# Kernel optimization log

Measured on AMD Instinct MI355X. Metric: run time of the kernel, lower is better.

## Reference

```python
import jax, jax.numpy as jnp
import numpy as np
from jax import lax

# Static problem sizes (see shape_source)
B, C, N = 32, 512, 64
SENTS_PER_VIDEO = 4
TARGETS_PER_SENT = 2
S = B * SENTS_PER_VIDEO          # 128 sentences
M = S * TARGETS_PER_SENT         # 256 target moments
P = N * (N + 1) // 2             # 2080 valid proposals (upper-tri mask2d)
T_TEMP = 0.1
MARGIN = 0.0
NEG_IOU = 0.5
K_TOP = 1                        # pos_topk
WEIGHT = 1.0


def setup_inputs() -> dict:
    key = jax.random.key(0)
    k1, k2, k3, k4 = jax.random.split(key, 4)
    return {
        "video_feats": jax.random.normal(k1, (B, C, N, N), jnp.float32),
        "sents_feats": jax.random.normal(k2, (S, C), jnp.float32),
        "num_sentences": jnp.full((B,), SENTS_PER_VIDEO, jnp.int32),
        "num_targets": jnp.full((S,), TARGETS_PER_SENT, jnp.int32),
        "iou2d": jax.random.uniform(k3, (S, N, N), jnp.float32),
        "iou2ds": jax.random.uniform(k4, (M, N, N), jnp.float32),
        "mask2d": jnp.triu(jnp.ones((N, N), bool)),
        "epoch": 0,  # < start_DNS_epoch -> DNS branch skipped
    }


def _log_cross_entropy(pos_scores, all_scores, neg_mask, t, m):
    # Faithful to LogCrossEntropy.forward
    pos_exp = jnp.exp((pos_scores - m) / t)
    neg_exp_sum = jnp.sum(jnp.exp(all_scores / t) * neg_mask, axis=-1)
    loss = -((pos_scores - m) / t - jnp.log(pos_exp + neg_exp_sum))
    return jnp.mean(loss)


def _l2_normalize(x, axis=-1, eps=1e-12):
    n = jnp.linalg.norm(x, axis=axis, keepdims=True)
    return x / jnp.maximum(n, eps)


def reference(video_feats, sents_feats, num_sentences, num_targets,
              iou2d, iou2ds, mask2d, epoch):
    # Compact valid proposals (P is static: upper-triangular mask2d)
    idx = jnp.nonzero(mask2d.reshape(-1), size=P)[0]              # (P,)
    v = video_feats.reshape(B, C, N * N)[:, :, idx]               # (B,C,P)
    v = jnp.transpose(v, (0, 2, 1))                               # (B,P,C)
    iou2d_f = iou2d.reshape(S, N * N)[:, idx]                     # (S,P)
    iou2ds_f = iou2ds.reshape(M, N * N)[:, idx]                   # (M,P)

    v = _l2_normalize(v)
    sents = _l2_normalize(sents_feats)

    scatter_s2v = jnp.repeat(jnp.arange(B), num_sentences, total_repeat_length=S)
    scatter_m2s = jnp.repeat(jnp.arange(S), num_targets, total_repeat_length=M)
    scatter_m2v = scatter_s2v[scatter_m2s]

    # top-K proposals per target moment by IoU
    topk_idx = lax.top_k(iou2ds_f, K_TOP)[1]                      # (M,K)
    topk_v = jnp.take_along_axis(v[scatter_m2v], topk_idx[:, :, None], axis=1)  # (M,K,C)

    # inter-video loss
    inter_video_pos = jnp.einsum('mkc,mc->mk', topk_v, sents[scatter_m2s])  # (M,K)
    inter_video_all = jnp.einsum('mkc,sc->mks', topk_v, sents)              # (M,K,S)
    inter_video_neg_mask = (~jnp.eye(S, dtype=bool))[scatter_m2s][:, None, :]  # (M,1,S)
    loss_inter_video = _log_cross_entropy(
        inter_video_pos, inter_video_all, inter_video_neg_mask, T_TEMP, MARGIN)

    # inter-query loss
    inter_query_pos = inter_video_pos                              # (M,K)
    inter_query_all = (sents @ v.reshape(B * P, C).T)[:, None, :]  # (S,1,B*P)
    # pos_mask: block-diagonal per video, refined by IoU > neg_iou inside own block
    onehot = jnp.eye(B, dtype=bool)[scatter_s2v]                   # (S,B)
    pos_mask = (onehot[:, :, None] & (iou2d_f > NEG_IOU)[:, None, :]).reshape(S, B * P)
    inter_query_neg_mask = (~pos_mask)[:, None, :]                 # (S,1,B*P)
    loss_inter_query = _log_cross_entropy(
        inter_query_pos, inter_query_all[scatter_m2s],
        inter_query_neg_mask[scatter_m2s], T_TEMP, MARGIN)

    total = (loss_inter_video + loss_inter_query) * WEIGHT
    return total, loss_inter_video, loss_inter_query
```

## Files before the change

kernel.cpp:

```cpp
#include <hip/hip_runtime.h>
#include <cstdint>

#define BB 32
#define CC 512
#define NSQ 4096
#define SS 128
#define MM 256
#define PP 2080

#define WS_SN     0
#define WS_SNB    262144
#define WS_IDX    393216
#define WS_IV     401536
#define WS_NEGQ   532608

typedef short bf16x8 __attribute__((ext_vector_type(8)));
typedef float f32x4  __attribute__((ext_vector_type(4)));

__device__ __forceinline__ unsigned short f2bf(float x) {
    unsigned int u = __float_as_uint(x);
    unsigned int r = (u + 0x7fffu + ((u >> 16) & 1u)) >> 16;
    return (unsigned short)r;
}

__global__ void k_prep(const float* __restrict__ sents, float* __restrict__ sn,
                       unsigned short* __restrict__ snb,
                       int* __restrict__ idx, float* __restrict__ negq) {
    const int blk = blockIdx.x, t = threadIdx.x;
    if (blk < 128) {
        __shared__ float red[256];
        const float* row = sents + (size_t)blk * CC;
        float x0 = row[t], x1 = row[t + 256];
        red[t] = x0 * x0 + x1 * x1;
        __syncthreads();
        for (int off = 128; off > 0; off >>= 1) {
            if (t < off) red[t] += red[t + off];
            __syncthreads();
        }
        float rn = 1.0f / fmaxf(sqrtf(red[0]), 1e-12f);
        float y0 = x0 * rn, y1 = x1 * rn;
        sn[(size_t)blk * CC + t]        = y0;
        sn[(size_t)blk * CC + t + 256]  = y1;
        snb[(size_t)blk * CC + t]       = f2bf(y0);
        snb[(size_t)blk * CC + t + 256] = f2bf(y1);
    } else if (blk < 144) {
        int i = (blk - 128) * 256 + t;
        int r = i >> 6, c = i & 63;
        if (c >= r) {
            int p = r * 64 - (r * (r - 1)) / 2 + (c - r);
            idx[p] = i;
        }
    } else {
        if (t < 128) negq[t] = 0.0f;
    }
}

#define BK 64
#define LDK 72

__global__ __launch_bounds__(256)
void k_bigd(const float* __restrict__ video, const unsigned short* __restrict__ snb,
            const float* __restrict__ iou2d, float* __restrict__ negq) {
    __shared__ char smem[36864];
    unsigned short* sA = (unsigned short*)smem;
    unsigned short* vB = (unsigned short*)(smem + 18432);

    const int t    = threadIdx.x;
    const int w    = t >> 6;
    const int lane = t & 63;
    const int q    = lane >> 4;
    const int l15  = lane & 15;

    const int b  = blockIdx.x >> 5;
    const int j0 = (blockIdx.x & 31) * 128;

    const int cg = t & 31;
    const int kr = t >> 5;

    f32x4 acc[2][8];
#pragma unroll
    for (int i = 0; i < 2; i++)
#pragma unroll
        for (int j = 0; j < 8; j++) acc[i][j] = (f32x4){0.f, 0.f, 0.f, 0.f};
    float sq0 = 0.f, sq1 = 0.f, sq2 = 0.f, sq3 = 0.f;

    for (int k0 = 0; k0 < CC; k0 += BK) {
        __syncthreads();
#pragma unroll
        for (int it = 0; it < 4; it++) {
            int lin = t + it * 256;
            int row = lin >> 3, kc = (lin & 7) * 8;
            bf16x8 v = *(const bf16x8*)(snb + (size_t)row * CC + k0 + kc);
            *(bf16x8*)(sA + row * LDK + kc) = v;
        }
        float4 r0[4], r1[4];
#pragma unroll
        for (int i = 0; i < 4; i++) {
            int k = 2 * (kr + 8 * i);
            const float* p = video + ((size_t)b * CC + k0 + k) * NSQ + j0 + 4 * cg;
            r0[i] = *(const float4*)p;
            r1[i] = *(const float4*)(p + NSQ);
        }
#pragma unroll
        for (int i = 0; i < 4; i++) {
            int kp = kr + 8 * i;
            sq0 += r0[i].x * r0[i].x + r1[i].x * r1[i].x;
            sq1 += r0[i].y * r0[i].y + r1[i].y * r1[i].y;
            sq2 += r0[i].z * r0[i].z + r1[i].z * r1[i].z;
            sq3 += r0[i].w * r0[i].w + r1[i].w * r1[i].w;
            unsigned int p0 = (unsigned int)f2bf(r0[i].x) | ((unsigned int)f2bf(r1[i].x) << 16);
            unsigned int p1 = (unsigned int)f2bf(r0[i].y) | ((unsigned int)f2bf(r1[i].y) << 16);
            unsigned int p2 = (unsigned int)f2bf(r0[i].z) | ((unsigned int)f2bf(r1[i].z) << 16);
            unsigned int p3 = (unsigned int)f2bf(r0[i].w) | ((unsigned int)f2bf(r1[i].w) << 16);
            *(unsigned int*)(vB + (4 * cg + 0) * LDK + 2 * kp) = p0;
            *(unsigned int*)(vB + (4 * cg + 1) * LDK + 2 * kp) = p1;
            *(unsigned int*)(vB + (4 * cg + 2) * LDK + 2 * kp) = p2;
            *(unsigned int*)(vB + (4 * cg + 3) * LDK + 2 * kp) = p3;
        }
        __syncthreads();
#pragma unroll
        for (int ks = 0; ks < BK; ks += 32) {
            bf16x8 a[2], bfr[8];
#pragma unroll
            for (int rt = 0; rt < 2; rt++) {
                int row = w * 32 + rt * 16 + l15;
                a[rt] = *(const bf16x8*)(sA + row * LDK + ks + q * 8);
            }
#pragma unroll
            for (int ct = 0; ct < 8; ct++) {
                int col = ct * 16 + l15;
                bfr[ct] = *(const bf16x8*)(vB + col * LDK + ks + q * 8);
            }
#pragma unroll
            for (int rt = 0; rt < 2; rt++)
#pragma unroll
                for (int ct = 0; ct < 8; ct++)
                    acc[rt][ct] = __builtin_amdgcn_mfma_f32_16x16x32_bf16(
                        a[rt], bfr[ct], acc[rt][ct], 0, 0, 0);
        }
    }
    __syncthreads();

    float* sqred = (float*)smem;
    float* redp  = (float*)(smem + 4608);
    float* colrn = (float*)(smem + 13312);

    sqred[(4 * cg + 0) * 9 + kr] = sq0;
    sqred[(4 * cg + 1) * 9 + kr] = sq1;
    sqred[(4 * cg + 2) * 9 + kr] = sq2;
    sqred[(4 * cg + 3) * 9 + kr] = sq3;
    __syncthreads();
    if (t < 128) {
        float ssum = 0.f;
#pragma unroll
        for (int x = 0; x < 8; x++) ssum += sqred[t * 9 + x];
        colrn[t] = 1.0f / fmaxf(sqrtf(ssum), 1e-12f);
    }
    __syncthreads();

#pragma unroll
    for (int rt = 0; rt < 2; rt++) {
#pragma unroll
        for (int r = 0; r < 4; r++) {
            int s = w * 32 + rt * 16 + q * 4 + r;
            bool myvid = ((s >> 2) == b);
            float rowsum = 0.f;
#pragma unroll
            for (int ct = 0; ct < 8; ct++) {
                int c = ct * 16 + l15;
                int j = j0 + c;
                bool valid = (j & 63) >= (j >> 6);
                float e = 0.f;
                if (valid) {
                    float sc = acc[rt][ct][r] * colrn[c];
                    e = expf(sc * 10.0f);
                    if (myvid && iou2d[(size_t)s * NSQ + j] > 0.5f) e = 0.f;
                }
                rowsum += e;
            }
            redp[s * 17 + l15] = rowsum;
        }
    }
    __syncthreads();
    if (t < 128) {
        float tot = 0.f;
#pragma unroll
        for (int x = 0; x < 16; x++) tot += redp[t * 17 + x];
        atomicAdd(&negq[t], tot);
    }
}

__global__ void k_fused(const float* __restrict__ video, const float* __restrict__ sn,
                        const float* __restrict__ iou2ds, const int* __restrict__ idx,
                        float* __restrict__ iv) {
    const int m = blockIdx.x, t = threadIdx.x;
    __shared__ float sv[256];
    __shared__ int   si[256];
    __shared__ float tvs[512];
    __shared__ float red[256];

    {
        float best = -1e30f; int bi = 1 << 30;
        const float* row = iou2ds + (size_t)m * NSQ;
        for (int p = t; p < PP; p += 256) {
            float v = row[idx[p]];
            if (v > best || (v == best && p < bi)) { best = v; bi = p; }
        }
        sv[t] = best; si[t] = bi;
        __syncthreads();
        for (int off = 128; off > 0; off >>= 1) {
            if (t < off) {
                float v2 = sv[t + off]; int i2 = si[t + off];
                if (v2 > sv[t] || (v2 == sv[t] && i2 < si[t])) { sv[t] = v2; si[t] = i2; }
            }
            __syncthreads();
        }
    }
    const int flat = idx[si[0]];
    const int b = m >> 3;

    const float* base = video + (size_t)b * CC * NSQ + flat;
    float x0 = base[(size_t)t * NSQ];
    float x1 = base[(size_t)(t + 256) * NSQ];
    red[t] = x0 * x0 + x1 * x1;
    __syncthreads();
    for (int off = 128; off > 0; off >>= 1) {
        if (t < off) red[t] += red[t + off];
        __syncthreads();
    }
    float rn = 1.0f / fmaxf(sqrtf(red[0]), 1e-12f);
    tvs[t] = x0 * rn;
    tvs[t + 256] = x1 * rn;
    __syncthreads();

    const int s = t & 127, h = t >> 7;
    const float4* a4 = (const float4*)(tvs + h * 256);
    const float4* b4 = (const float4*)(sn + (size_t)s * CC + h * 256);
    float acc = 0.f;
#pragma unroll 8
    for (int c = 0; c < 64; c++) {
        float4 a = a4[c], bb = b4[c];
        acc += a.x * bb.x + a.y * bb.y + a.z * bb.z + a.w * bb.w;
    }
    __syncthreads();
    red[t] = acc;
    __syncthreads();
    if (t < 128) iv[(size_t)m * SS + t] = red[t] + red[t + 128];
}

__global__ void k_final(const float* __restrict__ iv, const float* __restrict__ negq,
                        float* __restrict__ out) {
    const int t = threadIdx.x;
    __shared__ float rv[256], rq[256];
    const float* row = iv + (size_t)t * SS;
    const int ms = t >> 1;
    float pos = row[ms];
    float nv = 0.f;
    for (int s = 0; s < SS; s++) {
        float e = expf(row[s] * 10.0f);
        if (s == ms) e = 0.f;
        nv += e;
    }
    float pe = expf(pos * 10.0f);
    float lv = logf(pe + nv) - pos * 10.0f;
    float lq = logf(pe + negq[ms]) - pos * 10.0f;
    rv[t] = lv; rq[t] = lq;
    __syncthreads();
    for (int off = 128; off > 0; off >>= 1) {
        if (t < off) { rv[t] += rv[t + off]; rq[t] += rq[t + off]; }
        __syncthreads();
    }
    if (t == 0) {
        float liv = rv[0] / 256.f, liq = rq[0] / 256.f;
        out[0] = liv + liq;
        out[1] = liv;
        out[2] = liq;
    }
}

extern "C" void kernel_launch(void* const* d_in, const int* in_sizes, int n_in,
                              void* d_out, int out_size, void* d_ws, size_t ws_size,
                              hipStream_t stream) {
    const float* video  = (const float*)d_in[0];
    const float* sents  = (const float*)d_in[1];
    const float* iou2d  = (const float*)d_in[4];
    const float* iou2ds = (const float*)d_in[5];
    float* out = (float*)d_out;

    char* ws = (char*)d_ws;
    float*          sn   = (float*)(ws + WS_SN);
    unsigned short* snb  = (unsigned short*)(ws + WS_SNB);
    int*            idx  = (int*)(ws + WS_IDX);
    float*          iv   = (float*)(ws + WS_IV);
    float*          negq = (float*)(ws + WS_NEGQ);

    k_prep <<<145, 256, 0, stream>>>(sents, sn, snb, idx, negq);
    k_bigd <<<BB * 32, 256, 0, stream>>>(video, snb, iou2d, negq);
    k_fused<<<MM, 256, 0, stream>>>(video, sn, iou2ds, idx, iv);
    k_final<<<1, 256, 0, stream>>>(iv, negq, out);
}
```

Before: 421.0 us.

## Merge big GEMM and top-moment kernels into one launch, restructure video tile loads

New measurement: 420.4 us. About the same (-0.1%).

```diff
diff --git a/kernel.cpp b/kernel.cpp
--- a/kernel.cpp
+++ b/kernel.cpp
@@ -59,193 +59,183 @@
 #define LDK 72
 
 __global__ __launch_bounds__(256)
-void k_bigd(const float* __restrict__ video, const unsigned short* __restrict__ snb,
-            const float* __restrict__ iou2d, float* __restrict__ negq) {
+void k_big2(const float* __restrict__ video, const unsigned short* __restrict__ snb,
+            const float* __restrict__ sn, const float* __restrict__ iou2d,
+            const float* __restrict__ iou2ds, const int* __restrict__ idx,
+            float* __restrict__ negq, float* __restrict__ iv) {
     __shared__ char smem[36864];
-    unsigned short* sA = (unsigned short*)smem;
-    unsigned short* vB = (unsigned short*)(smem + 18432);
-
-    const int t    = threadIdx.x;
-    const int w    = t >> 6;
-    const int lane = t & 63;
-    const int q    = lane >> 4;
-    const int l15  = lane & 15;
-
-    const int b  = blockIdx.x >> 5;
-    const int j0 = (blockIdx.x & 31) * 128;
-
-    const int cg = t & 31;
-    const int kr = t >> 5;
-
-    f32x4 acc[2][8];
-#pragma unroll
-    for (int i = 0; i < 2; i++)
-#pragma unroll
-        for (int j = 0; j < 8; j++) acc[i][j] = (f32x4){0.f, 0.f, 0.f, 0.f};
-    float sq0 = 0.f, sq1 = 0.f, sq2 = 0.f, sq3 = 0.f;
-
-    for (int k0 = 0; k0 < CC; k0 += BK) {
-        __syncthreads();
-#pragma unroll
-        for (int it = 0; it < 4; it++) {
-            int lin = t + it * 256;
-            int row = lin >> 3, kc = (lin & 7) * 8;
-            bf16x8 v = *(const bf16x8*)(snb + (size_t)row * CC + k0 + kc);
-            *(bf16x8*)(sA + row * LDK + kc) = v;
-        }
-        float4 r0[4], r1[4];
-#pragma unroll
-        for (int i = 0; i < 4; i++) {
-            int k = 2 * (kr + 8 * i);
-            const float* p = video + ((size_t)b * CC + k0 + k) * NSQ + j0 + 4 * cg;
-            r0[i] = *(const float4*)p;
-            r1[i] = *(const float4*)(p + NSQ);
-        }
-#pragma unroll
-        for (int i = 0; i < 4; i++) {
-            int kp = kr + 8 * i;
-            sq0 += r0[i].x * r0[i].x + r1[i].x * r1[i].x;
-            sq1 += r0[i].y * r0[i].y + r1[i].y * r1[i].y;
-            sq2 += r0[i].z * r0[i].z + r1[i].z * r1[i].z;
-            sq3 += r0[i].w * r0[i].w + r1[i].w * r1[i].w;
-            unsigned int p0 = (unsigned int)f2bf(r0[i].x) | ((unsigned int)f2bf(r1[i].x) << 16);
-            unsigned int p1 = (unsigned int)f2bf(r0[i].y) | ((unsigned int)f2bf(r1[i].y) << 16);
-            unsigned int p2 = (unsigned int)f2bf(r0[i].z) | ((unsigned int)f2bf(r1[i].z) << 16);
-            unsigned int p3 = (unsigned int)f2bf(r0[i].w) | ((unsigned int)f2bf(r1[i].w) << 16);
-            *(unsigned int*)(vB + (4 * cg + 0) * LDK + 2 * kp) = p0;
-            *(unsigned int*)(vB + (4 * cg + 1) * LDK + 2 * kp) = p1;
-            *(unsigned int*)(vB + (4 * cg + 2) * LDK + 2 * kp) = p2;
-            *(unsigned int*)(vB + (4 * cg + 3) * LDK + 2 * kp) = p3;
-        }
-        __syncthreads();
-#pragma unroll
-        for (int ks = 0; ks < BK; ks += 32) {
-            bf16x8 a[2], bfr[8];
-#pragma unroll
-            for (int rt = 0; rt < 2; rt++) {
-                int row = w * 32 + rt * 16 + l15;
-                a[rt] = *(const bf16x8*)(sA + row * LDK + ks + q * 8);
-            }
-#pragma unroll
-            for (int ct = 0; ct < 8; ct++) {
-                int col = ct * 16 + l15;
-                bfr[ct] = *(const bf16x8*)(vB + col * LDK + ks + q * 8);
-            }
-#pragma unroll
-            for (int rt = 0; rt < 2; rt++)
-#pragma unroll
-                for (int ct = 0; ct < 8; ct++)
-                    acc[rt][ct] = __builtin_amdgcn_mfma_f32_16x16x32_bf16(
-                        a[rt], bfr[ct], acc[rt][ct], 0, 0, 0);
-        }
-    }
-    __syncthreads();
-
-    float* sqred = (float*)smem;
-    float* redp  = (float*)(smem + 4608);
-    float* colrn = (float*)(smem + 13312);
-
-    sqred[(4 * cg + 0) * 9 + kr] = sq0;
-    sqred[(4 * cg + 1) * 9 + kr] = sq1;
-    sqred[(4 * cg + 2) * 9 + kr] = sq2;
-    sqred[(4 * cg + 3) * 9 + kr] = sq3;
-    __syncthreads();
-    if (t < 128) {
-        float ssum = 0.f;
-#pragma unroll
-        for (int x = 0; x < 8; x++) ssum += sqred[t * 9 + x];
-        colrn[t] = 1.0f / fmaxf(sqrtf(ssum), 1e-12f);
-    }
-    __syncthreads();
-
-#pragma unroll
-    for (int rt = 0; rt < 2; rt++) {
-#pragma unroll
-        for (int r = 0; r < 4; r++) {
-            int s = w * 32 + rt * 16 + q * 4 + r;
-            bool myvid = ((s >> 2) == b);
-            float rowsum = 0.f;
-#pragma unroll
-            for (int ct = 0; ct < 8; ct++) {
-                int c = ct * 16 + l15;
-                int j = j0 + c;
-                bool valid = (j & 63) >= (j >> 6);
-                float e = 0.f;
-                if (valid) {
-                    float sc = acc[rt][ct][r] * colrn[c];
-                    e = expf(sc * 10.0f);
-                    if (myvid && iou2d[(size_t)s * NSQ + j] > 0.5f) e = 0.f;
-                }
-                rowsum += e;
-            }
-            redp[s * 17 + l15] = rowsum;
-        }
-    }
-    __syncthreads();
-    if (t < 128) {
-        float tot = 0.f;
-#pragma unroll
-        for (int x = 0; x < 16; x++) tot += redp[t * 17 + x];
-        atomicAdd(&negq[t], tot);
-    }
-}
-
-__global__ void k_fused(const float* __restrict__ video, const float* __restrict__ sn,
-                        const float* __restrict__ iou2ds, const int* __restrict__ idx,
-                        float* __restrict__ iv) {
-    const int m = blockIdx.x, t = threadIdx.x;
-    __shared__ float sv[256];
-    __shared__ int   si[256];
-    __shared__ float tvs[512];
-    __shared__ float red[256];
-
-    {
-        float best = -1e30f; int bi = 1 << 30;
-        const float* row = iou2ds + (size_t)m * NSQ;
-        for (int p = t; p < PP; p += 256) {
-            float v = row[idx[p]];
-            if (v > best || (v == best && p < bi)) { best = v; bi = p; }
-        }
-        sv[t] = best; si[t] = bi;
+    const int t = threadIdx.x;
+
+    if (blockIdx.x < 1024) {
+        unsigned short* sA = (unsigned short*)smem;
+        unsigned short* vB = (unsigned short*)(smem + 18432);
+
+        const int w    = t >> 6;
+        const int lane = t & 63;
+        const int q    = lane >> 4;
+        const int l15  = lane & 15;
+
+        const int b  = blockIdx.x >> 5;
+        const int j0 = (blockIdx.x & 31) * 128;
+
+        const int jj = t & 127;
+        const int kh = t >> 7;
+
+        f32x4 acc[2][8];
+#pragma unroll
+        for (int i = 0; i < 2; i++)
+#pragma unroll
+            for (int j = 0; j < 8; j++) acc[i][j] = (f32x4){0.f, 0.f, 0.f, 0.f};
+        float sq = 0.f;
+
+        const float* vcol = video + (size_t)b * CC * NSQ + j0 + jj;
+
+        for (int k0 = 0; k0 < CC; k0 += BK) {
+            __syncthreads();
+#pragma unroll
+            for (int it = 0; it < 4; it++) {
+                int lin = t + it * 256;
+                int row = lin >> 3, kc = (lin & 7) * 8;
+                bf16x8 v = *(const bf16x8*)(snb + (size_t)row * CC + k0 + kc);
+                *(bf16x8*)(sA + row * LDK + kc) = v;
+            }
+            const float* vp = vcol + (size_t)(k0 + kh * 32) * NSQ;
+#pragma unroll
+            for (int h = 0; h < 2; h++) {
+                float x[16];
+#pragma unroll
+                for (int i = 0; i < 16; i++) x[i] = vp[(size_t)(h * 16 + i) * NSQ];
+#pragma unroll
+                for (int g = 0; g < 2; g++) {
+                    alignas(16) unsigned short buf[8];
+#pragma unroll
+                    for (int i = 0; i < 8; i++) {
+                        float v = x[g * 8 + i];
+                        sq += v * v;
+                        buf[i] = f2bf(v);
+                    }
+                    *(bf16x8*)(vB + jj * LDK + kh * 32 + h * 16 + g * 8) = *(bf16x8*)buf;
+                }
+            }
+            __syncthreads();
+#pragma unroll
+            for (int ks = 0; ks < BK; ks += 32) {
+                bf16x8 a[2], bfr[8];
+#pragma unroll
+                for (int rt = 0; rt < 2; rt++) {
+                    int row = w * 32 + rt * 16 + l15;
+                    a[rt] = *(const bf16x8*)(sA + row * LDK + ks + q * 8);
+                }
+#pragma unroll
+                for (int ct = 0; ct < 8; ct++) {
+                    int col = ct * 16 + l15;
+                    bfr[ct] = *(const bf16x8*)(vB + col * LDK + ks + q * 8);
+                }
+#pragma unroll
+                for (int rt = 0; rt < 2; rt++)
+#pragma unroll
+                    for (int ct = 0; ct < 8; ct++)
+                        acc[rt][ct] = __builtin_amdgcn_mfma_f32_16x16x32_bf16(
+                            a[rt], bfr[ct], acc[rt][ct], 0, 0, 0);
+            }
+        }
+        __syncthreads();
+
+        float* sqred = (float*)smem;
+        float* redp  = (float*)(smem + 2048);
+        float* colrn = (float*)(smem + 11264);
+
+        sqred[jj * 3 + kh] = sq;
+        __syncthreads();
+        if (t < 128)
+            colrn[t] = 1.0f / fmaxf(sqrtf(sqred[t * 3] + sqred[t * 3 + 1]), 1e-12f);
+        __syncthreads();
+
+#pragma unroll
+        for (int rt = 0; rt < 2; rt++) {
+#pragma unroll
+            for (int r = 0; r < 4; r++) {
+                int s = w * 32 + rt * 16 + q * 4 + r;
+                bool myvid = ((s >> 2) == b);
+                float rowsum = 0.f;
+#pragma unroll
+                for (int ct = 0; ct < 8; ct++) {
+                    int c = ct * 16 + l15;
+                    int j = j0 + c;
+                    bool valid = (j & 63) >= (j >> 6);
+                    float e = 0.f;
+                    if (valid) {
+                        float sc = acc[rt][ct][r] * colrn[c];
+                        e = expf(sc * 10.0f);
+                        if (myvid && iou2d[(size_t)s * NSQ + j] > 0.5f) e = 0.f;
+                    }
+                    rowsum += e;
+                }
+                redp[s * 17 + l15] = rowsum;
+            }
+        }
+        __syncthreads();
+        if (t < 128) {
+            float tot = 0.f;
+#pragma unroll
+            for (int x = 0; x < 16; x++) tot += redp[t * 17 + x];
+            atomicAdd(&negq[t], tot);
+        }
+    } else {
+        const int m = blockIdx.x - 1024;
+        float* sv  = (float*)smem;
+        int*   si  = (int*)(smem + 1024);
+        float* tvs = (float*)(smem + 2048);
+        float* red = (float*)(smem + 4096);
+
+        {
+            float best = -1e30f; int bi = 1 << 30;
+            const float* row = iou2ds + (size_t)m * NSQ;
+            for (int p = t; p < PP; p += 256) {
+                float v = row[idx[p]];
+                if (v > best || (v == best && p < bi)) { best = v; bi = p; }
+            }
+            sv[t] = best; si[t] = bi;
+            __syncthreads();
+            for (int off = 128; off > 0; off >>= 1) {
+                if (t < off) {
+                    float v2 = sv[t + off]; int i2 = si[t + off];
+                    if (v2 > sv[t] || (v2 == sv[t] && i2 < si[t])) { sv[t] = v2; si[t] = i2; }
+                }
+                __syncthreads();
+            }
+        }
+        const int flat = idx[si[0]];
+        const int b = m >> 3;
+
+        const float* base = video + (size_t)b * CC * NSQ + flat;
+        float x0 = base[(size_t)t * NSQ];
+        float x1 = base[(size_t)(t + 256) * NSQ];
+        red[t] = x0 * x0 + x1 * x1;
         __syncthreads();
         for (int off = 128; off > 0; off >>= 1) {
-            if (t < off) {
-                float v2 = sv[t + off]; int i2 = si[t + off];
-                if (v2 > sv[t] || (v2 == sv[t] && i2 < si[t])) { sv[t] = v2; si[t] = i2; }
-            }
-            __syncthreads();
-        }
-    }
-    const int flat = idx[si[0]];
-    const int b = m >> 3;
-
-    const float* base = video + (size_t)b * CC * NSQ + flat;
-    float x0 = base[(size_t)t * NSQ];
-    float x1 = base[(size_t)(t + 256) * NSQ];
-    red[t] = x0 * x0 + x1 * x1;
-    __syncthreads();
-    for (int off = 128; off > 0; off >>= 1) {
-        if (t < off) red[t] += red[t + off];
-        __syncthreads();
-    }
-    float rn = 1.0f / fmaxf(sqrtf(red[0]), 1e-12f);
-    tvs[t] = x0 * rn;
-    tvs[t + 256] = x1 * rn;
-    __syncthreads();
-
-    const int s = t & 127, h = t >> 7;
-    const float4* a4 = (const float4*)(tvs + h * 256);
-    const float4* b4 = (const float4*)(sn + (size_t)s * CC + h * 256);
-    float acc = 0.f;
+            if (t < off) red[t] += red[t + off];
+            __syncthreads();
+        }
+        float rn = 1.0f / fmaxf(sqrtf(red[0]), 1e-12f);
+        tvs[t] = x0 * rn;
+        tvs[t + 256] = x1 * rn;
+        __syncthreads();
+
+        const int s = t & 127, h = t >> 7;
+        const float4* a4 = (const float4*)(tvs + h * 256);
+        const float4* b4 = (const float4*)(sn + (size_t)s * CC + h * 256);
+        float acc2 = 0.f;
 #pragma unroll 8
-    for (int c = 0; c < 64; c++) {
-        float4 a = a4[c], bb = b4[c];
-        acc += a.x * bb.x + a.y * bb.y + a.z * bb.z + a.w * bb.w;
-    }
-    __syncthreads();
-    red[t] = acc;
-    __syncthreads();
-    if (t < 128) iv[(size_t)m * SS + t] = red[t] + red[t + 128];
+        for (int c = 0; c < 64; c++) {
+            float4 a = a4[c], bb = b4[c];
+            acc2 += a.x * bb.x + a.y * bb.y + a.z * bb.z + a.w * bb.w;
+        }
+        __syncthreads();
+        red[t] = acc2;
+        __syncthreads();
+        if (t < 128) iv[(size_t)m * SS + t] = red[t] + red[t + 128];
+    }
 }
 
 __global__ void k_final(const float* __restrict__ iv, const float* __restrict__ negq,
@@ -295,7 +285,6 @@
     float*          negq = (float*)(ws + WS_NEGQ);
 
     k_prep <<<145, 256, 0, stream>>>(sents, sn, snb, idx, negq);
-    k_bigd <<<BB * 32, 256, 0, stream>>>(video, snb, iou2d, negq);
-    k_fused<<<MM, 256, 0, stream>>>(video, sn, iou2ds, idx, iv);
+    k_big2 <<<1024 + MM, 256, 0, stream>>>(video, snb, sn, iou2d, iou2ds, idx, negq, iv);
     k_final<<<1, 256, 0, stream>>>(iv, negq, out);
 }
```
